# Kernel optimization log

Hardware: AMD Instinct MI355X
Metric: run time of the kernel (lower is better)

The kernel has to match this reference:

```python
import jax, jax.numpy as jnp
import numpy as np

B, T, D, H, L, C = 64, 512, 256, 1024, 2, 128


def setup_inputs() -> dict:
    key = jax.random.key(0)
    ks = jax.random.split(key, 11)
    s = 0.05
    return {
        "x": jax.random.normal(ks[0], (B, T, D), dtype=jnp.float32),
        "W_ih0": jax.random.normal(ks[1], (4 * H, D), dtype=jnp.float32) * s,
        "W_hh0": jax.random.normal(ks[2], (4 * H, H), dtype=jnp.float32) * s,
        "b_ih0": jax.random.normal(ks[3], (4 * H,), dtype=jnp.float32) * s,
        "b_hh0": jax.random.normal(ks[4], (4 * H,), dtype=jnp.float32) * s,
        "W_ih1": jax.random.normal(ks[5], (4 * H, H), dtype=jnp.float32) * s,
        "W_hh1": jax.random.normal(ks[6], (4 * H, H), dtype=jnp.float32) * s,
        "b_ih1": jax.random.normal(ks[7], (4 * H,), dtype=jnp.float32) * s,
        "b_hh1": jax.random.normal(ks[8], (4 * H,), dtype=jnp.float32) * s,
        "W_fc": jax.random.normal(ks[9], (C, H), dtype=jnp.float32) * s,
        "b_fc": jax.random.normal(ks[10], (C,), dtype=jnp.float32) * s,
    }


def _lstm_cell(inp, h, c, Wi, Wh, bi, bh):
    # PyTorch LSTMCell: gates ordered i, f, g, o
    gates = inp @ Wi.T + bi + h @ Wh.T + bh  # [B, 4H]
    i, f, g, o = jnp.split(gates, 4, axis=-1)
    c_new = jax.nn.sigmoid(f) * c + jax.nn.sigmoid(i) * jnp.tanh(g)
    h_new = jax.nn.sigmoid(o) * jnp.tanh(c_new)
    return h_new, c_new


def reference(x, W_ih0, W_hh0, b_ih0, b_hh0, W_ih1, W_hh1, b_ih1, b_hh1, W_fc, b_fc):
    b = x.shape[0]
    h0 = jnp.zeros((b, H), x.dtype)
    init = (h0, h0, h0, h0)  # (h_l0, c_l0, h_l1, c_l1)

    def step(carry, x_t):
        h0_, c0_, h1_, c1_ = carry
        h0n, c0n = _lstm_cell(x_t, h0_, c0_, W_ih0, W_hh0, b_ih0, b_hh0)
        h1n, c1n = _lstm_cell(h0n, h1_, c1_, W_ih1, W_hh1, b_ih1, b_hh1)
        return (h0n, c0n, h1n, c1n), None

    xt = jnp.swapaxes(x, 0, 1)  # [T, B, D]
    (h0f, c0f, h1f, c1f), _ = jax.lax.scan(step, init, xt)
    return h1f @ W_fc.T + b_fc  # [B, num_classes]
```

## Files before the change

kernel.cpp:

```cpp
#include <hip/hip_runtime.h>
#include <hip/hip_bf16.h>

#define B_ 64
#define T_ 512
#define D_ 256
#define H_ 1024
#define RING 64
#define PS 260

typedef __attribute__((ext_vector_type(8))) short short8;
typedef __attribute__((ext_vector_type(4))) float floatx4;

__device__ __forceinline__ unsigned short f2bf(float f){
  unsigned u = __builtin_bit_cast(unsigned, f);
  u = (u + 0x7fffu + ((u >> 16) & 1u)) >> 16;
  return (unsigned short)u;
}

__device__ __forceinline__ short8 pack8(floatx4 a, floatx4 b){
  short8 r;
  r[0]=(short)f2bf(a[0]); r[1]=(short)f2bf(a[1]); r[2]=(short)f2bf(a[2]); r[3]=(short)f2bf(a[3]);
  r[4]=(short)f2bf(b[0]); r[5]=(short)f2bf(b[1]); r[6]=(short)f2bf(b[2]); r[7]=(short)f2bf(b[3]);
  return r;
}

__device__ __forceinline__ float sigm(float v){ return 1.f/(1.f+__expf(-v)); }
__device__ __forceinline__ float tanh_f(float v){ return 1.f - 2.f/(1.f+__expf(2.f*v)); }

__device__ __forceinline__ void gpoll(const unsigned long long* watch, unsigned tgt0, unsigned tgt1){
  if (!(tgt0 | tgt1)) return;
  long g = 0;
  for (;;){
    unsigned long long v = __hip_atomic_load(watch, __ATOMIC_RELAXED, __HIP_MEMORY_SCOPE_AGENT);
    unsigned v0 = (unsigned)v, v1 = (unsigned)(v >> 32);
    if (__all(v0 >= tgt0 && v1 >= tgt1)) break;
    if (++g > (1L<<24)) break;
  }
}

__device__ __forceinline__ void lspin(unsigned* flag, unsigned tgt){
  long g = 0;
  while (__hip_atomic_load(flag, __ATOMIC_RELAXED, __HIP_MEMORY_SCOPE_WORKGROUP) < tgt){
    if (++g > (1L<<24)) break;
  }
}


template<int LAYER>
__device__ __forceinline__ void run_lstm(
    const float* __restrict__ x,
    const float* __restrict__ Wi, const float* __restrict__ Wh,
    const float* __restrict__ bi, const float* __restrict__ bh,
    unsigned* seq, unsigned short* h0h, unsigned short* h1h, float* h1f,
    int jbase, int j, int half,
    float* partial , float* c_st , float* biasv ,
    unsigned* rdy )
{
  constexpr int KTOT = LAYER ? 2048 : 1280;
  constexpr int KW   = KTOT/8;
  constexpr int NK   = KW/32;
  constexpr int KA   = LAYER ? 1024 : 256;

  const int tid  = threadIdx.x;
  const int wave = tid >> 6;
  const int lane = tid & 63;
  const int ksl  = wave;
  const int n15  = lane & 15;
  const int kq   = (lane >> 4) * 8;

  short8 bfr[4][NK];
  #pragma unroll
  for (int nt = 0; nt < 4; nt++){
    int n   = nt*16 + n15;
    int row = (n >> 4)*H_ + jbase + (n & 15);
    #pragma unroll
    for (int ks = 0; ks < NK; ks++){
      int k = ksl*KW + ks*32 + kq;
      const float* s = (k < KA) ? (Wi + (size_t)row*KA + k)
                                : (Wh + (size_t)row*H_ + (k - KA));
      bfr[nt][ks] = pack8(*(const floatx4*)s, *(const floatx4*)(s + 4));
    }
  }
  if (tid < 64){
    int col = (tid >> 4)*H_ + jbase + (tid & 15);
    biasv[tid] = bi[col] + bh[col];
  }
  c_st[tid & 511] = 0.f;
  if (tid == 0){ rdy[0] = 0u; rdy[1] = 0u; }
  __syncthreads();

  const unsigned long long* watch = (const unsigned long long*)seq + (half*64 + lane);

  for (int t = 0; t < T_; t++){
    floatx4 xraw[LAYER ? 1 : NK][2][2];
    if constexpr (LAYER == 0){
      #pragma unroll
      for (int ks = 0; ks < NK; ks++){
        const int kb = ksl*KW + ks*32;
        if (kb < D_){
          const int kk = kb + kq;
          #pragma unroll
          for (int mt = 0; mt < 2; mt++){
            const float* xs = x + ((size_t)(half*32 + mt*16 + n15)*T_ + t)*D_ + kk;
            xraw[ks][mt][0] = *(const floatx4*)xs;
            xraw[ks][mt][1] = *(const floatx4*)(xs + 4);
          }
        }
      }
    }

    if (LAYER == 0){
      if (wave == 0){
        gpoll(watch, 0u, (t >= RING) ? (unsigned)(t - RING + 1) : 0u);
      } else if (wave == 1){
        gpoll(watch, (unsigned)t, 0u);
        if (lane == 0) __hip_atomic_store(&rdy[0], (unsigned)(t + 1),
                                          __ATOMIC_RELAXED, __HIP_MEMORY_SCOPE_WORKGROUP);
      } else {
        lspin(&rdy[0], (unsigned)(t + 1));
      }
    } else {
      if (wave == 0){
        gpoll(watch, (unsigned)(t + 1), 0u);
        if (lane == 0) __hip_atomic_store(&rdy[0], (unsigned)(t + 1),
                                          __ATOMIC_RELAXED, __HIP_MEMORY_SCOPE_WORKGROUP);
      } else if (wave < 4){
        lspin(&rdy[0], (unsigned)(t + 1));
      } else if (wave == 4){
        gpoll(watch, 0u, (unsigned)t);
        if (lane == 0) __hip_atomic_store(&rdy[1], (unsigned)(t + 1),
                                          __ATOMIC_RELAXED, __HIP_MEMORY_SCOPE_WORKGROUP);
      } else {
        lspin(&rdy[1], (unsigned)(t + 1));
      }
    }
    __builtin_amdgcn_sched_barrier(0);

    floatx4 acc[2][4];
    #pragma unroll
    for (int mt = 0; mt < 2; mt++)
      #pragma unroll
      for (int nt = 0; nt < 4; nt++)
        acc[mt][nt] = (floatx4)0.f;

    const unsigned short* h0t = h0h + ((size_t)((LAYER ? t : (t-1)) & (RING-1)) << 16);
    const unsigned short* h1t = h1h + ((size_t)((t-1) & (RING-1)) << 16);

    #pragma unroll
    for (int ks = 0; ks < NK; ks++){
      const int kb = ksl*KW + ks*32;
      if (kb >= KA && t == 0) continue;
      const int kk = kb + kq;
      short8 afr[2];
      if constexpr (LAYER == 0){
        if (kb < D_){
          #pragma unroll
          for (int mt = 0; mt < 2; mt++)
            afr[mt] = pack8(xraw[ks][mt][0], xraw[ks][mt][1]);
        } else {
          const int hk = kk - D_;
          const unsigned short* p = h0t + ((hk >> 4) << 10) + (hk & 15);
          #pragma unroll
          for (int mt = 0; mt < 2; mt++)
            afr[mt] = *(const short8*)(p + ((half*32 + mt*16 + n15) << 4));
        }
      } else {
        const int hk = (kb < 1024) ? kk : (kk - 1024);
        const unsigned short* sb = (kb < 1024) ? h0t : h1t;
        const unsigned short* p = sb + ((hk >> 4) << 10) + (hk & 15);
        #pragma unroll
        for (int mt = 0; mt < 2; mt++)
          afr[mt] = *(const short8*)(p + ((half*32 + mt*16 + n15) << 4));
      }
      #pragma unroll
      for (int mt = 0; mt < 2; mt++)
        #pragma unroll
        for (int nt = 0; nt < 4; nt++)
          acc[mt][nt] = __builtin_amdgcn_mfma_f32_16x16x32_bf16(afr[mt], bfr[nt][ks], acc[mt][nt], 0, 0, 0);
    }

    #pragma unroll
    for (int mt = 0; mt < 2; mt++)
      #pragma unroll
      for (int nt = 0; nt < 4; nt++){
        int n  = nt*16 + n15;
        int b0 = mt*16 + (lane >> 4)*4;
        *(floatx4*)(partial + (size_t)n*PS + ksl*32 + b0) = acc[mt][nt];
      }
    __syncthreads();

    {
      int b = tid >> 4, jj = tid & 15;
      float g[4];
      #pragma unroll
      for (int q = 0; q < 4; q++){
        const float* p = partial + (size_t)(q*16 + jj)*PS + b;
        float s = biasv[q*16 + jj];
        #pragma unroll
        for (int ss = 0; ss < 8; ss++) s += p[ss*32];
        g[q] = s;
      }
      float co = c_st[tid];
      float si = sigm(g[0]), sf = sigm(g[1]), tg = tanh_f(g[2]), so = sigm(g[3]);
      float cn = sf*co + si*tg;
      float hn = so*tanh_f(cn);
      c_st[tid] = cn;
      unsigned hb = (unsigned)f2bf(hn);
      unsigned ob = (unsigned)__shfl_xor((int)hb, 1, 64);
      if (!(jj & 1)){
        unsigned pk = hb | (ob << 16);
        unsigned short* dst = (LAYER ? h1h : h0h)
                            + ((size_t)(t & (RING-1)) << 16)
                            + ((size_t)j << 10) + ((size_t)(half*32 + b) << 4) + jj;
        __hip_atomic_store((unsigned*)dst, pk, __ATOMIC_RELAXED, __HIP_MEMORY_SCOPE_AGENT);
      }
      if (LAYER == 1 && t == T_-1)
        h1f[(size_t)(half*32 + b)*H_ + jbase + jj] = hn;
    }
    __syncthreads();
    if (tid == 0)
      __hip_atomic_store(seq + (size_t)(half*64 + j)*2 + LAYER, (unsigned)(t + 1),
                         __ATOMIC_RELAXED, __HIP_MEMORY_SCOPE_AGENT);
  }
}

__global__ __launch_bounds__(512, 2) void lstm_pk(
    const float* __restrict__ x,
    const float* __restrict__ Wih0, const float* __restrict__ Whh0,
    const float* __restrict__ bih0, const float* __restrict__ bhh0,
    const float* __restrict__ Wih1, const float* __restrict__ Whh1,
    const float* __restrict__ bih1, const float* __restrict__ bhh1,
    char* __restrict__ ws)
{
  __shared__ __align__(16) float partial[64*PS];
  __shared__ float c_st[512];
  __shared__ float biasv[64];
  __shared__ unsigned rdy[2];

  unsigned* seq       = (unsigned*)ws;
  unsigned short* h0h = (unsigned short*)(ws + (1<<20));
  unsigned short* h1h = (unsigned short*)(ws + (1<<20) + RING*B_*H_*2);
  float* h1f          = (float*)(ws + (1<<20) + 2*(size_t)RING*B_*H_*2);

  const int bid = blockIdx.x;
  if (bid < 128){
    run_lstm<0>(x, Wih0, Whh0, bih0, bhh0, seq, h0h, h1h, h1f,
                (bid & 63)*16, bid & 63, bid >> 6, partial, c_st, biasv, rdy);
  } else {
    const int r = bid - 128;
    run_lstm<1>(x, Wih1, Whh1, bih1, bhh1, seq, h0h, h1h, h1f,
                (r & 63)*16, r & 63, r >> 6, partial, c_st, biasv, rdy);
  }
}

__global__ __launch_bounds__(128) void fc_k(
    const float* __restrict__ h1f, const float* __restrict__ Wfc,
    const float* __restrict__ bfc, float* __restrict__ out)
{
  __shared__ float hv[1024];
  int b = blockIdx.x, c = threadIdx.x;
  for (int i = c; i < 1024; i += 128) hv[i] = h1f[(size_t)b*1024 + i];
  __syncthreads();
  const floatx4* w4 = (const floatx4*)(Wfc + (size_t)c*1024);
  const floatx4* h4 = (const floatx4*)hv;
  float acc = 0.f;
  #pragma unroll 8
  for (int k = 0; k < 256; k++){
    floatx4 wv = w4[k];
    floatx4 hh = h4[k];
    acc += wv[0]*hh[0] + wv[1]*hh[1] + wv[2]*hh[2] + wv[3]*hh[3];
  }
  out[(size_t)b*128 + c] = acc + bfc[c];
}

extern "C" void kernel_launch(void* const* d_in, const int* in_sizes, int n_in,
                              void* d_out, int out_size, void* d_ws, size_t ws_size,
                              hipStream_t stream)
{
  const float* x    = (const float*)d_in[0];
  const float* Wih0 = (const float*)d_in[1];
  const float* Whh0 = (const float*)d_in[2];
  const float* bih0 = (const float*)d_in[3];
  const float* bhh0 = (const float*)d_in[4];
  const float* Wih1 = (const float*)d_in[5];
  const float* Whh1 = (const float*)d_in[6];
  const float* bih1 = (const float*)d_in[7];
  const float* bhh1 = (const float*)d_in[8];
  const float* Wfc  = (const float*)d_in[9];
  const float* bfc  = (const float*)d_in[10];

  hipMemsetAsync(d_ws, 0, 128*2*sizeof(unsigned), stream);

  lstm_pk<<<256, 512, 0, stream>>>(x, Wih0, Whh0, bih0, bhh0, Wih1, Whh1, bih1, bhh1, (char*)d_ws);

  const float* h1f = (const float*)((char*)d_ws + (1<<20) + 2*(size_t)RING*B_*H_*2);
  fc_k<<<64, 128, 0, stream>>>(h1f, Wfc, bfc, (float*)d_out);
}
```

Measured before the change: 3.117 ms.

## Replicate step flags per layer so one wave polls a single cache line

```diff
diff --git a/kernel.cpp b/kernel.cpp
--- a/kernel.cpp
+++ b/kernel.cpp
@@ -54,7 +54,7 @@
     unsigned* seq, unsigned short* h0h, unsigned short* h1h, float* h1f,
     int jbase, int j, int half,
     float* partial , float* c_st , float* biasv ,
-    unsigned* rdy )
+    unsigned* rdy)
 {
   constexpr int KTOT = LAYER ? 2048 : 1280;
   constexpr int KW   = KTOT/8;
@@ -86,10 +86,13 @@
     biasv[tid] = bi[col] + bh[col];
   }
   c_st[tid & 511] = 0.f;
-  if (tid == 0){ rdy[0] = 0u; rdy[1] = 0u; }
+  if (tid == 0){ rdy[0] = 0u; }
   __syncthreads();
 
-  const unsigned long long* watch = (const unsigned long long*)seq + (half*64 + lane);
+  const unsigned long long* watch =
+      (const unsigned long long*)seq + (size_t)(LAYER*2 + half)*512 + lane;
+  unsigned* post0 = seq + (size_t)(0*2 + half)*1024 + (size_t)j*2 + LAYER;
+  unsigned* post1 = seq + (size_t)(1*2 + half)*1024 + (size_t)j*2 + LAYER;
 
   for (int t = 0; t < T_; t++){
     floatx4 xraw[LAYER ? 1 : NK][2][2];
@@ -109,30 +112,20 @@
       }
     }
 
-    if (LAYER == 0){
-      if (wave == 0){
-        gpoll(watch, 0u, (t >= RING) ? (unsigned)(t - RING + 1) : 0u);
-      } else if (wave == 1){
-        gpoll(watch, (unsigned)t, 0u);
-        if (lane == 0) __hip_atomic_store(&rdy[0], (unsigned)(t + 1),
-                                          __ATOMIC_RELAXED, __HIP_MEMORY_SCOPE_WORKGROUP);
+    if (wave == 0){
+      unsigned tgt0, tgt1;
+      if (LAYER == 0){
+        tgt0 = (unsigned)t;
+        tgt1 = (t >= RING) ? (unsigned)(t - RING + 1) : 0u;
       } else {
-        lspin(&rdy[0], (unsigned)(t + 1));
-      }
+        tgt0 = (unsigned)(t + 1);
+        tgt1 = (unsigned)t;
+      }
+      gpoll(watch, tgt0, tgt1);
+      if (lane == 0) __hip_atomic_store(&rdy[0], (unsigned)(t + 1),
+                                        __ATOMIC_RELAXED, __HIP_MEMORY_SCOPE_WORKGROUP);
     } else {
-      if (wave == 0){
-        gpoll(watch, (unsigned)(t + 1), 0u);
-        if (lane == 0) __hip_atomic_store(&rdy[0], (unsigned)(t + 1),
-                                          __ATOMIC_RELAXED, __HIP_MEMORY_SCOPE_WORKGROUP);
-      } else if (wave < 4){
-        lspin(&rdy[0], (unsigned)(t + 1));
-      } else if (wave == 4){
-        gpoll(watch, 0u, (unsigned)t);
-        if (lane == 0) __hip_atomic_store(&rdy[1], (unsigned)(t + 1),
-                                          __ATOMIC_RELAXED, __HIP_MEMORY_SCOPE_WORKGROUP);
-      } else {
-        lspin(&rdy[1], (unsigned)(t + 1));
-      }
+      lspin(&rdy[0], (unsigned)(t + 1));
     }
     __builtin_amdgcn_sched_barrier(0);
 
@@ -218,9 +211,10 @@
         h1f[(size_t)(half*32 + b)*H_ + jbase + jj] = hn;
     }
     __syncthreads();
-    if (tid == 0)
-      __hip_atomic_store(seq + (size_t)(half*64 + j)*2 + LAYER, (unsigned)(t + 1),
-                         __ATOMIC_RELAXED, __HIP_MEMORY_SCOPE_AGENT);
+    if (tid == 0){
+      __hip_atomic_store(post0, (unsigned)(t + 1), __ATOMIC_RELAXED, __HIP_MEMORY_SCOPE_AGENT);
+      __hip_atomic_store(post1, (unsigned)(t + 1), __ATOMIC_RELAXED, __HIP_MEMORY_SCOPE_AGENT);
+    }
   }
 }
 
@@ -235,7 +229,7 @@
   __shared__ __align__(16) float partial[64*PS];
   __shared__ float c_st[512];
   __shared__ float biasv[64];
-  __shared__ unsigned rdy[2];
+  __shared__ unsigned rdy[1];
 
   unsigned* seq       = (unsigned*)ws;
   unsigned short* h0h = (unsigned short*)(ws + (1<<20));
@@ -289,7 +283,7 @@
   const float* Wfc  = (const float*)d_in[9];
   const float* bfc  = (const float*)d_in[10];
 
-  hipMemsetAsync(d_ws, 0, 128*2*sizeof(unsigned), stream);
+  hipMemsetAsync(d_ws, 0, 4*4096, stream);
 
   lstm_pk<<<256, 512, 0, stream>>>(x, Wih0, Whh0, bih0, bhh0, Wih1, Whh1, bih1, bhh1, (char*)d_ws);
 
```

Result: slower. 3.342 ms (+7.2%).
